# Performance work log

Hardware: AMD Instinct MI355X
Metric: run time of the kernel (lower is better)

The kernel has to match this reference:

```python
import jax, jax.numpy as jnp
import numpy as np
from math import sqrt

I = 1024  # input_size
H = 1024  # hidden_size
B = 4096  # batch


def setup_inputs() -> dict:
    key = jax.random.key(0)
    ks = jax.random.split(key, 12)
    a = 1.0 / sqrt(H)
    u = lambda k, shape: jax.random.uniform(k, shape, jnp.float32, -a, a)
    return {
        "x": jax.random.normal(ks[0], (B, I), jnp.float32),
        "hx": jax.random.normal(ks[1], (B, H), jnp.float32),
        "cx": jax.random.normal(ks[2], (B, H), jnp.float32),
        "weight_ih": u(ks[3], (4 * H, I)),
        "weight_hh": u(ks[4], (4 * H, H)),
        "bias_ih": u(ks[5], (4 * H,)),
        "bias_hh": u(ks[6], (4 * H,)),
        "W_peephole_i": u(ks[7], (H, H)),
        "W_peephole_f": u(ks[8], (H, H)),
        "W_peephole_o": u(ks[9], (H, H)),
    }


def reference(x, hx, cx, weight_ih, weight_hh, bias_ih, bias_hh,
              W_peephole_i, W_peephole_f, W_peephole_o):
    # gates: [B, 4H]
    gates = x @ weight_ih.T + bias_ih + hx @ weight_hh.T + bias_hh
    ingate, forgetgate, cellgate, outgate = jnp.split(gates, 4, axis=1)
    # F.linear(cx, W * eye) == cx * diag(W)  (diagonal peephole)
    ingate = jax.nn.sigmoid(ingate + cx * jnp.diagonal(W_peephole_i))
    forgetgate = jax.nn.sigmoid(forgetgate + cx * jnp.diagonal(W_peephole_f))
    cellgate = jnp.tanh(cellgate)
    cy = forgetgate * cx + ingate * cellgate
    # NOTE: original code reuses W_peephole_f for the output gate (faithful to source)
    outgate = jax.nn.sigmoid(outgate + cy * jnp.diagonal(W_peephole_f))
    hy = outgate * jnp.tanh(cy)
    return (hy, cy)
```

## Files before the change

kernel.cpp:

```cpp
#include <hip/hip_runtime.h>
#include <cstdint>


namespace {

constexpr int H   = 1024;
constexpr int K2  = 2048;
constexpr int BSZ = 4096;
constexpr size_t OUT_CY = (size_t)BSZ * H;

typedef __attribute__((ext_vector_type(8))) short bf16x8;
typedef __attribute__((ext_vector_type(4))) float f32x4;
typedef __attribute__((ext_vector_type(8))) unsigned short u16x8;

__device__ __forceinline__ unsigned short f2bf(float f) {
  union { float f; uint32_t u; } v; v.f = f;
  uint32_t u = v.u;
  u += 0x7FFFu + ((u >> 16) & 1u);
  return (unsigned short)(u >> 16);
}

__device__ __forceinline__ float sigm(float x) {
  return 1.0f / (1.0f + __expf(-x));
}
__device__ __forceinline__ float tanh_fast(float x) {
  return 1.0f - 2.0f / (1.0f + __expf(2.0f * x));
}

__device__ __forceinline__ void gload_lds16(const void* g, void* l) {
  __builtin_amdgcn_global_load_lds(
      (const __attribute__((address_space(1))) void*)g,
      (__attribute__((address_space(3))) void*)l, 16, 0, 0);
}

__device__ __forceinline__ bf16x8 dsr_b128(unsigned addr) {
  bf16x8 r;
  asm volatile("ds_read_b128 %0, %1" : "=v"(r) : "v"(addr));
  return r;
}

}

__global__ __launch_bounds__(256) void cast_kernel(
    const float* __restrict__ x, const float* __restrict__ hx,
    const float* __restrict__ wih, const float* __restrict__ whh,
    unsigned short* __restrict__ A, unsigned short* __restrict__ W) {
  int b = blockIdx.x;
  bool isW = b >= 4096;
  int t = (isW ? b - 4096 : b) * 256 + threadIdx.x;
  int idx = t * 8;
  int n = idx >> 11;
  int k = idx & 2047;
  const float* s0 = isW ? wih : x;
  const float* s1 = isW ? whh : hx;
  const float* src = (k < H) ? (s0 + (size_t)n * H + k)
                             : (s1 + (size_t)n * H + (k - H));
  float4 v0 = *(const float4*)src;
  float4 v1 = *(const float4*)(src + 4);
  u16x8 o;
  o[0] = f2bf(v0.x); o[1] = f2bf(v0.y); o[2] = f2bf(v0.z); o[3] = f2bf(v0.w);
  o[4] = f2bf(v1.x); o[5] = f2bf(v1.y); o[6] = f2bf(v1.z); o[7] = f2bf(v1.w);
  if (isW) {
    int g = n >> 10, hh = n & 1023;
    int np = ((hh >> 4) << 6) + (g << 4) + (hh & 15);
    *(u16x8*)(W + (size_t)np * K2 + k) = o;
  } else {
    *(u16x8*)(A + (size_t)idx) = o;
  }
}

#define RD_A(AF, Q, BO)                                            \
  AF[0][0] = dsr_b128(abase + (BO) + (2 * (Q) + 0) * 2048 + kch0); \
  AF[0][1] = dsr_b128(abase + (BO) + (2 * (Q) + 0) * 2048 + kch1); \
  AF[1][0] = dsr_b128(abase + (BO) + (2 * (Q) + 1) * 2048 + kch0); \
  AF[1][1] = dsr_b128(abase + (BO) + (2 * (Q) + 1) * 2048 + kch1);

#define MFMA_PH(Q, AF, BC)                                                   \
  __builtin_amdgcn_s_setprio(1);                                             \
  _Pragma("unroll") for (int i2 = 0; i2 < 2; ++i2)                           \
      _Pragma("unroll") for (int j = 0; j < 4; ++j)                          \
          acc[2 * (Q) + i2][j] = __builtin_amdgcn_mfma_f32_16x16x32_bf16(    \
              AF[i2][0], BC[j][0], acc[2 * (Q) + i2][j], 0, 0, 0);           \
  _Pragma("unroll") for (int i2 = 0; i2 < 2; ++i2)                           \
      _Pragma("unroll") for (int j = 0; j < 4; ++j)                          \
          acc[2 * (Q) + i2][j] = __builtin_amdgcn_mfma_f32_16x16x32_bf16(    \
              AF[i2][1], BC[j][1], acc[2 * (Q) + i2][j], 0, 0, 0);           \
  __builtin_amdgcn_s_setprio(0);

#define LGKM(N)                                           \
  asm volatile("s_waitcnt lgkmcnt(" #N ")" ::: "memory"); \
  __builtin_amdgcn_sched_barrier(0);

#define TILE_BODY(KT, BUF)                                                   \
  {                                                                          \
    const unsigned bo = (BUF) * 65536u;                                      \
    bf16x8 bfr[4][2], af0[2][2], af1[2][2];                                  \
    _Pragma("unroll") for (int j = 0; j < 4; ++j) {                          \
      bfr[j][0] = dsr_b128(bbase + bo + j * 2048 + kch0);                    \
      bfr[j][1] = dsr_b128(bbase + bo + j * 2048 + kch1);                    \
    }                                                                        \
    RD_A(af0, 0, bo);                                                        \
    RD_A(af1, 1, bo);                                    \
    LGKM(4);                             \
    MFMA_PH(0, af0, bfr);                                                    \
    RD_A(af0, 2, bo);                                                        \
    LGKM(4);                                  \
    MFMA_PH(1, af1, bfr);                                                    \
    RD_A(af1, 3, bo);                                                        \
    LGKM(4);                                   \
    MFMA_PH(2, af0, bfr);                                                    \
    LGKM(0);                 \
    MFMA_PH(3, af1, bfr);                                                    \
    __builtin_amdgcn_s_barrier();  \
    if ((KT) + 2 < 32) {                                                     \
      stA((KT) + 2, (BUF), 0); stA((KT) + 2, (BUF), 1);                      \
      stA((KT) + 2, (BUF), 2); stA((KT) + 2, (BUF), 3);                      \
      stB((KT) + 2, (BUF), 0); stB((KT) + 2, (BUF), 1);                      \
      stB((KT) + 2, (BUF), 2); stB((KT) + 2, (BUF), 3);                      \
      asm volatile("s_waitcnt vmcnt(8)" ::: "memory");      \
    } else {                                                                 \
      asm volatile("s_waitcnt vmcnt(0)" ::: "memory");       \
    }                                                                        \
    __builtin_amdgcn_sched_barrier(0);                                       \
    __builtin_amdgcn_s_barrier();    \
  }

__global__ __launch_bounds__(512, 2) void lstm_fused_gemm(
    const unsigned short* __restrict__ A,
    const unsigned short* __restrict__ W,
    const float* __restrict__ cx,
    const float* __restrict__ bias_ih, const float* __restrict__ bias_hh,
    const float* __restrict__ Wpi, const float* __restrict__ Wpf,
    float* __restrict__ out) {
  __shared__ __align__(16) unsigned short lds[2 * 32768];

  const int tid  = threadIdx.x;
  const int lane = tid & 63;
  const int wave = tid >> 6;
  const int wm   = wave >> 2;
  const int wn   = wave & 3;

  const int b   = blockIdx.y * 16 + blockIdx.x;
  const int xcd = b & 7, bidx = b >> 3;
  const int bx  = (xcd & 3) * 4 + (bidx & 3);
  const int by  = (xcd >> 2) * 8 + (bidx >> 2);
  const int m0 = bx * 256;
  const int w0 = by * 256;

  const int srow   = tid >> 3;
  const int schunk = ((tid & 7) ^ (srow & 7)) << 3;

  const int col  = lane & 15;
  const int quad = lane >> 4;

  const unsigned short* Asrc = A + (size_t)(m0 + srow) * K2 + schunk;
  const unsigned short* Wsrc = W + (size_t)(w0 + srow) * K2 + schunk;
  const int ldsdst = wave * 512;

  f32x4 acc[8][4];
#pragma unroll
  for (int i = 0; i < 8; ++i)
#pragma unroll
    for (int j = 0; j < 4; ++j)
      acc[i][j] = (f32x4){0.f, 0.f, 0.f, 0.f};

  auto stA = [&](int kt, int buf, int p) {
    gload_lds16(Asrc + (size_t)p * 64 * K2 + kt * 64,
                &lds[buf * 32768 + p * 4096 + ldsdst]);
  };
  auto stB = [&](int kt, int buf, int p) {
    gload_lds16(Wsrc + (size_t)p * 64 * K2 + kt * 64,
                &lds[buf * 32768 + 16384 + p * 4096 + ldsdst]);
  };

  const unsigned lds0 = (unsigned)(size_t)(__attribute__((address_space(3))) char*)lds;
  const unsigned abase = lds0 + (unsigned)((wm * 128 + col) * 128);
  const unsigned bbase = lds0 + 32768u + (unsigned)((wn * 64 + col) * 128);
  const unsigned kch0 = ((quad ^ (col & 7)) << 4);
  const unsigned kch1 = (((4 + quad) ^ (col & 7)) << 4);

#pragma unroll
  for (int p = 0; p < 4; ++p) stA(0, 0, p);
#pragma unroll
  for (int p = 0; p < 4; ++p) stB(0, 0, p);
#pragma unroll
  for (int p = 0; p < 4; ++p) stA(1, 1, p);
#pragma unroll
  for (int p = 0; p < 4; ++p) stB(1, 1, p);
  asm volatile("s_waitcnt vmcnt(8)" ::: "memory");
  __builtin_amdgcn_sched_barrier(0);
  __builtin_amdgcn_s_barrier();

  for (int kt = 0; kt < 32; kt += 2) {
    TILE_BODY(kt, 0);
    TILE_BODY(kt + 1, 1);
  }

  const int h = by * 64 + wn * 16 + col;
  const float bi  = bias_ih[h]         + bias_hh[h];
  const float bf_ = bias_ih[H + h]     + bias_hh[H + h];
  const float bc  = bias_ih[2 * H + h] + bias_hh[2 * H + h];
  const float bo_ = bias_ih[3 * H + h] + bias_hh[3 * H + h];
  const float di = Wpi[(size_t)h * (H + 1)];
  const float df = Wpf[(size_t)h * (H + 1)];
  const int mbase = m0 + wm * 128 + quad * 4;
#pragma unroll
  for (int i = 0; i < 8; ++i) {
#pragma unroll
    for (int r = 0; r < 4; ++r) {
      const int m = mbase + i * 16 + r;
      const float c  = cx[(size_t)m * H + h];
      const float ip = acc[i][0][r] + bi;
      const float fp = acc[i][1][r] + bf_;
      const float cp = acc[i][2][r] + bc;
      const float op = acc[i][3][r] + bo_;
      const float ig = sigm(ip + c * di);
      const float fg = sigm(fp + c * df);
      const float cg = tanh_fast(cp);
      const float cy = fg * c + ig * cg;
      const float og = sigm(op + cy * df);
      const float hy = og * tanh_fast(cy);
      out[(size_t)m * H + h] = hy;
      out[OUT_CY + (size_t)m * H + h] = cy;
    }
  }
}

extern "C" void kernel_launch(void* const* d_in, const int* in_sizes, int n_in,
                              void* d_out, int out_size, void* d_ws, size_t ws_size,
                              hipStream_t stream) {
  const float* x   = (const float*)d_in[0];
  const float* hx  = (const float*)d_in[1];
  const float* cx  = (const float*)d_in[2];
  const float* wih = (const float*)d_in[3];
  const float* whh = (const float*)d_in[4];
  const float* bih = (const float*)d_in[5];
  const float* bhh = (const float*)d_in[6];
  const float* wpi = (const float*)d_in[7];
  const float* wpf = (const float*)d_in[8];
  float* out = (float*)d_out;

  unsigned short* Abf = (unsigned short*)d_ws;
  unsigned short* Wbf = Abf + (size_t)BSZ * K2;

  cast_kernel<<<8192, 256, 0, stream>>>(x, hx, wih, whh, Abf, Wbf);

  dim3 grid(BSZ / 256, (4 * H) / 256);
  lstm_fused_gemm<<<grid, 512, 0, stream>>>(Abf, Wbf, cx, bih, bhh, wpi, wpf, out);
}
```

Measured before the change: 247.2 us.

## Switch GEMM to 32x32x16 MFMA with 4x2 wave tiling and interleaved loads

Result: faster. 210.3 us (-14.9%).

```diff
diff --git a/kernel.cpp b/kernel.cpp
--- a/kernel.cpp
+++ b/kernel.cpp
@@ -10,7 +10,7 @@
 constexpr size_t OUT_CY = (size_t)BSZ * H;
 
 typedef __attribute__((ext_vector_type(8))) short bf16x8;
-typedef __attribute__((ext_vector_type(4))) float f32x4;
+typedef __attribute__((ext_vector_type(16))) float f32x16;
 typedef __attribute__((ext_vector_type(8))) unsigned short u16x8;
 
 __device__ __forceinline__ unsigned short f2bf(float f) {
@@ -62,67 +62,79 @@
   o[4] = f2bf(v1.x); o[5] = f2bf(v1.y); o[6] = f2bf(v1.z); o[7] = f2bf(v1.w);
   if (isW) {
     int g = n >> 10, hh = n & 1023;
-    int np = ((hh >> 4) << 6) + (g << 4) + (hh & 15);
+    int np = ((hh >> 5) << 7) + (g << 5) + (hh & 31);
     *(u16x8*)(W + (size_t)np * K2 + k) = o;
   } else {
     *(u16x8*)(A + (size_t)idx) = o;
   }
 }
 
-#define RD_A(AF, Q, BO)                                            \
-  AF[0][0] = dsr_b128(abase + (BO) + (2 * (Q) + 0) * 2048 + kch0); \
-  AF[0][1] = dsr_b128(abase + (BO) + (2 * (Q) + 0) * 2048 + kch1); \
-  AF[1][0] = dsr_b128(abase + (BO) + (2 * (Q) + 1) * 2048 + kch0); \
-  AF[1][1] = dsr_b128(abase + (BO) + (2 * (Q) + 1) * 2048 + kch1);
-
-#define MFMA_PH(Q, AF, BC)                                                   \
-  __builtin_amdgcn_s_setprio(1);                                             \
-  _Pragma("unroll") for (int i2 = 0; i2 < 2; ++i2)                           \
-      _Pragma("unroll") for (int j = 0; j < 4; ++j)                          \
-          acc[2 * (Q) + i2][j] = __builtin_amdgcn_mfma_f32_16x16x32_bf16(    \
-              AF[i2][0], BC[j][0], acc[2 * (Q) + i2][j], 0, 0, 0);           \
-  _Pragma("unroll") for (int i2 = 0; i2 < 2; ++i2)                           \
-      _Pragma("unroll") for (int j = 0; j < 4; ++j)                          \
-          acc[2 * (Q) + i2][j] = __builtin_amdgcn_mfma_f32_16x16x32_bf16(    \
-              AF[i2][1], BC[j][1], acc[2 * (Q) + i2][j], 0, 0, 0);           \
+#define RD_B(BB, Q, BO)                                  \
+  BB[0] = dsr_b128(bbase + (BO) + (Q) * 4096 + kc0);     \
+  BB[1] = dsr_b128(bbase + (BO) + (Q) * 4096 + kc1);     \
+  BB[2] = dsr_b128(bbase + (BO) + (Q) * 4096 + kc2);     \
+  BB[3] = dsr_b128(bbase + (BO) + (Q) * 4096 + kc3);
+
+#define MFMA_PH(Q, AF, BB)                                                 \
+  __builtin_amdgcn_s_setprio(1);                                           \
+  _Pragma("unroll") for (int kq = 0; kq < 4; ++kq)                         \
+      _Pragma("unroll") for (int i2 = 0; i2 < 2; ++i2)                     \
+          acc[i2][(Q)] = __builtin_amdgcn_mfma_f32_32x32x16_bf16(          \
+              AF[i2][kq], BB[kq], acc[i2][(Q)], 0, 0, 0);                  \
   __builtin_amdgcn_s_setprio(0);
 
-#define LGKM(N)                                           \
-  asm volatile("s_waitcnt lgkmcnt(" #N ")" ::: "memory"); \
+#define LGKM0                                            \
+  asm volatile("s_waitcnt lgkmcnt(0)" ::: "memory");     \
   __builtin_amdgcn_sched_barrier(0);
 
 #define TILE_BODY(KT, BUF)                                                   \
   {                                                                          \
     const unsigned bo = (BUF) * 65536u;                                      \
-    bf16x8 bfr[4][2], af0[2][2], af1[2][2];                                  \
-    _Pragma("unroll") for (int j = 0; j < 4; ++j) {                          \
-      bfr[j][0] = dsr_b128(bbase + bo + j * 2048 + kch0);                    \
-      bfr[j][1] = dsr_b128(bbase + bo + j * 2048 + kch1);                    \
+    bf16x8 a[2][4], bb[4];                                                   \
+                     \
+    _Pragma("unroll") for (int i2 = 0; i2 < 2; ++i2) {                       \
+      a[i2][0] = dsr_b128(abase + bo + i2 * 4096 + kc0);                     \
+      a[i2][1] = dsr_b128(abase + bo + i2 * 4096 + kc1);                     \
+      a[i2][2] = dsr_b128(abase + bo + i2 * 4096 + kc2);                     \
+      a[i2][3] = dsr_b128(abase + bo + i2 * 4096 + kc3);                     \
     }                                                                        \
-    RD_A(af0, 0, bo);                                                        \
-    RD_A(af1, 1, bo);                                    \
-    LGKM(4);                             \
-    MFMA_PH(0, af0, bfr);                                                    \
-    RD_A(af0, 2, bo);                                                        \
-    LGKM(4);                                  \
-    MFMA_PH(1, af1, bfr);                                                    \
-    RD_A(af1, 3, bo);                                                        \
-    LGKM(4);                                   \
-    MFMA_PH(2, af0, bfr);                                                    \
-    LGKM(0);                 \
-    MFMA_PH(3, af1, bfr);                                                    \
-    __builtin_amdgcn_s_barrier();  \
+    RD_B(bb, 0, bo);                                                         \
+    __builtin_amdgcn_s_barrier();                                            \
+    LGKM0;                                                                   \
+    MFMA_PH(0, a, bb);                                                       \
+    __builtin_amdgcn_s_barrier();                                            \
+             \
+    RD_B(bb, 1, bo);                                                         \
+    if ((KT) + 2 < 32) { stA((KT) + 2, (BUF), 0); stA((KT) + 2, (BUF), 1); } \
+    __builtin_amdgcn_s_barrier();                                            \
+    LGKM0;                                                                   \
+    MFMA_PH(1, a, bb);                                                       \
+    __builtin_amdgcn_s_barrier();                                            \
+                                  \
+    RD_B(bb, 2, bo);                                                         \
+    if ((KT) + 2 < 32) { stA((KT) + 2, (BUF), 2); stA((KT) + 2, (BUF), 3); } \
+    __builtin_amdgcn_s_barrier();                                            \
+    LGKM0;                                                                   \
+    MFMA_PH(2, a, bb);                                                       \
+    __builtin_amdgcn_s_barrier();                                            \
+             \
+    RD_B(bb, 3, bo);                                                         \
+    if ((KT) + 2 < 32) { stB((KT) + 2, (BUF), 0); stB((KT) + 2, (BUF), 2); } \
+    __builtin_amdgcn_s_barrier();                                            \
+    LGKM0;                                                                   \
+    MFMA_PH(3, a, bb);                                                       \
+    __builtin_amdgcn_s_barrier();                                            \
+      \
+      \
+      \
     if ((KT) + 2 < 32) {                                                     \
-      stA((KT) + 2, (BUF), 0); stA((KT) + 2, (BUF), 1);                      \
-      stA((KT) + 2, (BUF), 2); stA((KT) + 2, (BUF), 3);                      \
-      stB((KT) + 2, (BUF), 0); stB((KT) + 2, (BUF), 1);                      \
-      stB((KT) + 2, (BUF), 2); stB((KT) + 2, (BUF), 3);                      \
-      asm volatile("s_waitcnt vmcnt(8)" ::: "memory");      \
+      stB((KT) + 2, (BUF), 1); stB((KT) + 2, (BUF), 3);                      \
+      asm volatile("s_waitcnt vmcnt(8)" ::: "memory");                       \
     } else {                                                                 \
-      asm volatile("s_waitcnt vmcnt(0)" ::: "memory");       \
+      asm volatile("s_waitcnt vmcnt(0)" ::: "memory");                       \
     }                                                                        \
     __builtin_amdgcn_sched_barrier(0);                                       \
-    __builtin_amdgcn_s_barrier();    \
+    __builtin_amdgcn_s_barrier();                                            \
   }
 
 __global__ __launch_bounds__(512, 2) void lstm_fused_gemm(
@@ -137,8 +149,8 @@
   const int tid  = threadIdx.x;
   const int lane = tid & 63;
   const int wave = tid >> 6;
-  const int wm   = wave >> 2;
-  const int wn   = wave & 3;
+  const int wm   = wave >> 1;
+  const int wn   = wave & 1;
 
   const int b   = blockIdx.y * 16 + blockIdx.x;
   const int xcd = b & 7, bidx = b >> 3;
@@ -150,19 +162,16 @@
   const int srow   = tid >> 3;
   const int schunk = ((tid & 7) ^ (srow & 7)) << 3;
 
-  const int col  = lane & 15;
-  const int quad = lane >> 4;
-
   const unsigned short* Asrc = A + (size_t)(m0 + srow) * K2 + schunk;
   const unsigned short* Wsrc = W + (size_t)(w0 + srow) * K2 + schunk;
   const int ldsdst = wave * 512;
 
-  f32x4 acc[8][4];
-#pragma unroll
-  for (int i = 0; i < 8; ++i)
+  f32x16 acc[2][4];
+#pragma unroll
+  for (int i = 0; i < 2; ++i)
 #pragma unroll
     for (int j = 0; j < 4; ++j)
-      acc[i][j] = (f32x4){0.f, 0.f, 0.f, 0.f};
+      acc[i][j] = (f32x16)(0.f);
 
   auto stA = [&](int kt, int buf, int p) {
     gload_lds16(Asrc + (size_t)p * 64 * K2 + kt * 64,
@@ -174,10 +183,13 @@
   };
 
   const unsigned lds0 = (unsigned)(size_t)(__attribute__((address_space(3))) char*)lds;
-  const unsigned abase = lds0 + (unsigned)((wm * 128 + col) * 128);
-  const unsigned bbase = lds0 + 32768u + (unsigned)((wn * 64 + col) * 128);
-  const unsigned kch0 = ((quad ^ (col & 7)) << 4);
-  const unsigned kch1 = (((4 + quad) ^ (col & 7)) << 4);
+  const unsigned abase = lds0 + (unsigned)((wm * 64 + (lane & 31)) * 128);
+  const unsigned bbase = lds0 + 32768u + (unsigned)((wn * 128 + (lane & 31)) * 128);
+  const int l5 = lane >> 5, l7 = lane & 7;
+  const unsigned kc0 = (unsigned)(((0 + l5) ^ l7) << 4);
+  const unsigned kc1 = (unsigned)(((2 + l5) ^ l7) << 4);
+  const unsigned kc2 = (unsigned)(((4 + l5) ^ l7) << 4);
+  const unsigned kc3 = (unsigned)(((6 + l5) ^ l7) << 4);
 
 #pragma unroll
   for (int p = 0; p < 4; ++p) stA(0, 0, p);
@@ -196,19 +208,19 @@
     TILE_BODY(kt + 1, 1);
   }
 
-  const int h = by * 64 + wn * 16 + col;
+  const int h = by * 64 + wn * 32 + (lane & 31);
   const float bi  = bias_ih[h]         + bias_hh[h];
   const float bf_ = bias_ih[H + h]     + bias_hh[H + h];
   const float bc  = bias_ih[2 * H + h] + bias_hh[2 * H + h];
   const float bo_ = bias_ih[3 * H + h] + bias_hh[3 * H + h];
   const float di = Wpi[(size_t)h * (H + 1)];
   const float df = Wpf[(size_t)h * (H + 1)];
-  const int mbase = m0 + wm * 128 + quad * 4;
-#pragma unroll
-  for (int i = 0; i < 8; ++i) {
-#pragma unroll
-    for (int r = 0; r < 4; ++r) {
-      const int m = mbase + i * 16 + r;
+  const int mbase = m0 + wm * 64 + l5 * 4;
+#pragma unroll
+  for (int i = 0; i < 2; ++i) {
+#pragma unroll
+    for (int r = 0; r < 16; ++r) {
+      const int m = mbase + i * 32 + (r & 3) + 8 * (r >> 2);
       const float c  = cx[(size_t)m * H + h];
       const float ip = acc[i][0][r] + bi;
       const float fp = acc[i][1][r] + bf_;
```
